# Optimization experiments

Measured on AMD Instinct MI355X. Metric: run time of the kernel, lower is better.

The kernel has to match this reference:

```python
import jax, jax.numpy as jnp
import numpy as np

GAMMA = 10.0  # params[('edge_penalty_gamma', 10.0, ...)]
EPS_SQRT = 1e-24  # guard for sqrt(0) (float_aware_sqrt)


def dXf(u, dx):
    # forward difference along axis -2, Neumann-zero boundary (replicate last row)
    return (jnp.concatenate([u[..., 1:, :], u[..., -1:, :]], axis=-2) - u) / dx


def dYf(u, dy):
    # forward difference along axis -1, Neumann-zero boundary (replicate last col)
    return (jnp.concatenate([u[..., :, 1:], u[..., :, -1:]], axis=-1) - u) / dy


def setup_inputs() -> dict:
    key = jax.random.key(0)
    k1, k2 = jax.random.split(key)
    B, K, H, W = 8, 8, 1024, 1024
    input_images = jax.random.normal(k1, (B, 1, H, W), dtype=jnp.float32)
    spacing = jnp.ones((2,), dtype=jnp.float32)
    label_probabilities = jax.random.uniform(k2, (B, K, H, W), dtype=jnp.float32)
    return {"input_images": input_images, "spacing": spacing,
            "label_probabilities": label_probabilities}


def reference(input_images, spacing, label_probabilities):
    # --- compute_localized_edge_penalty(I, spacing) ---
    I = input_images[:, 0, ...]                      # [B, H, W]
    sx, sy = spacing[0], spacing[1]
    gn2 = dXf(I, sx) ** 2 + dYf(I, sy) ** 2          # ||grad I||^2 (forward diffs)
    gnI = jnp.sqrt(jnp.maximum(gn2, EPS_SQRT))
    w_edge = 1.0 / (1.0 + GAMMA * gnI * jnp.min(spacing))  # [B, H, W]

    # --- normalized-cut relaxation over all clusters, fully batched ---
    p = label_probabilities                          # [B, K, H, W]
    # cut-cost stencil uses unit spacing (fd.FD_torch(spacing=[1.0]*dim))
    p_xp = dXf(p, 1.0)
    p_yp = dYf(p, 1.0)
    w = w_edge[:, None, :, :]                        # broadcast over clusters
    nom = jnp.sum(p * (p + w * (p_xp + p_yp)), axis=(-2, -1))   # [B, K]
    denom = jnp.sum(p * (1.0 + 2.0 * w), axis=(-2, -1))         # [B, K]
    cut_cost = nom / denom                                        # [B, K]

    B, K = p.shape[0], p.shape[1]
    current_penalties = K - jnp.sum(cut_cost, axis=1)            # [B]
    return jnp.sum(current_penalties)
```

## Files before the change

kernel.cpp:

```cpp
#include <hip/hip_runtime.h>


constexpr int Bsz  = 8;
constexpr int Kc   = 8;
constexpr int KPB  = 4;
constexpr int H    = 1024;
constexpr int W    = 1024;
constexpr int ROWS = 16;
constexpr int RB   = H / ROWS;
constexpr int TPB  = 256;

#define GAMMA_F    10.0f
#define EPS_SQRT_F 1e-24f

__device__ __forceinline__ float wedge(float c, float dn, float rt,
                                       float inv_sx, float inv_sy, float smin) {
    float dx = (dn - c) * inv_sx;
    float dy = (rt - c) * inv_sy;
    float gn2 = dx * dx + dy * dy;
    float g = sqrtf(fmaxf(gn2, EPS_SQRT_F));
    return 1.0f / (1.0f + GAMMA_F * g * smin);
}

__device__ __forceinline__ void accum(float pc, float pd, float pr, float w,
                                      float& nom, float& den) {
    float lap = (pd - pc) + (pr - pc);
    nom = fmaf(pc, fmaf(w, lap, pc), nom);
    den = fmaf(pc, fmaf(2.0f, w, 1.0f), den);
}

__global__ __launch_bounds__(TPB) void cl_main(const float* __restrict__ I,
                                               const float* __restrict__ spacing,
                                               const float* __restrict__ P,
                                               float2* __restrict__ ws) {
    const int t    = threadIdx.x;
    const int lane = t & 63;
    const int j0   = t * 4;
    const int b    = blockIdx.y;
    const int kh   = blockIdx.z;
    const int r0   = blockIdx.x * ROWS;

    const float sx = spacing[0], sy = spacing[1];
    const float inv_sx = 1.0f / sx, inv_sy = 1.0f / sy;
    const float smin = fminf(sx, sy);

    const int jr = (j0 + 4 < W) ? (j0 + 4) : (W - 1);
    const bool edge = (lane == 63);

    const float* Ib = I + (size_t)b * H * W;
    const float* Pk0 = P + ((size_t)(b * Kc + kh * KPB)) * H * W;

    float4 cI  = *(const float4*)(Ib + (size_t)r0 * W + j0);
    float  cIr = edge ? Ib[(size_t)r0 * W + jr] : 0.0f;
    float4 cp[KPB];
    float  cpr[KPB];
#pragma unroll
    for (int k = 0; k < KPB; ++k) {
        const float* Pk = Pk0 + (size_t)k * H * W;
        cp[k]  = *(const float4*)(Pk + (size_t)r0 * W + j0);
        cpr[k] = edge ? Pk[(size_t)r0 * W + jr] : 0.0f;
    }

    float nom[KPB], den[KPB];
#pragma unroll
    for (int k = 0; k < KPB; ++k) { nom[k] = 0.0f; den[k] = 0.0f; }

#pragma unroll 1
    for (int ii = 0; ii < ROWS; ++ii) {
        const int i = r0 + ii;
        const int inext = (i + 1 < H) ? (i + 1) : (H - 1);
        const size_t rn = (size_t)inext * W;

        const float4 nI  = *(const float4*)(Ib + rn + j0);
        const float  nIr = edge ? Ib[rn + jr] : 0.0f;

        float Irt = __shfl_down(cI.x, 1, 64);
        if (edge) Irt = cIr;

        const float w0 = wedge(cI.x, nI.x, cI.y, inv_sx, inv_sy, smin);
        const float w1 = wedge(cI.y, nI.y, cI.z, inv_sx, inv_sy, smin);
        const float w2 = wedge(cI.z, nI.z, cI.w, inv_sx, inv_sy, smin);
        const float w3 = wedge(cI.w, nI.w, Irt,  inv_sx, inv_sy, smin);

#pragma unroll
        for (int k = 0; k < KPB; ++k) {
            const float* Pk = Pk0 + (size_t)k * H * W;
            const float4 np  = *(const float4*)(Pk + rn + j0);
            const float  npr = edge ? Pk[rn + jr] : 0.0f;

            float prt = __shfl_down(cp[k].x, 1, 64);
            if (edge) prt = cpr[k];

            accum(cp[k].x, np.x, cp[k].y, w0, nom[k], den[k]);
            accum(cp[k].y, np.y, cp[k].z, w1, nom[k], den[k]);
            accum(cp[k].z, np.z, cp[k].w, w2, nom[k], den[k]);
            accum(cp[k].w, np.w, prt,     w3, nom[k], den[k]);

            cp[k]  = np;
            cpr[k] = npr;
        }
        cI  = nI;
        cIr = nIr;
    }

    __shared__ float red[4][2 * KPB];
    const int wave = t >> 6;

#pragma unroll
    for (int k = 0; k < KPB; ++k) {
        float n = nom[k], d = den[k];
#pragma unroll
        for (int off = 32; off > 0; off >>= 1) {
            n += __shfl_down(n, off, 64);
            d += __shfl_down(d, off, 64);
        }
        if (lane == 0) {
            red[wave][k]       = n;
            red[wave][KPB + k] = d;
        }
    }
    __syncthreads();

    if (t < KPB) {
        const int k = t;
        float n = red[0][k] + red[1][k] + red[2][k] + red[3][k];
        float d = red[0][KPB + k] + red[1][KPB + k] + red[2][KPB + k] + red[3][KPB + k];
        ws[(((size_t)(b * 2 + kh) * RB) + blockIdx.x) * KPB + k] = make_float2(n, d);
    }
}

__global__ __launch_bounds__(512) void cl_final(const float2* __restrict__ ws,
                                                float* __restrict__ out) {
    const int t    = threadIdx.x;
    const int acc  = t & 63;
    const int part = t >> 6;
    const int b = acc >> 3, k = acc & 7;
    const int kh = k >> 2, kk = k & 3;

    double n = 0.0, d = 0.0;
#pragma unroll
    for (int r = part; r < RB; r += 8) {
        const float2 v = ws[(((size_t)(b * 2 + kh) * RB) + r) * KPB + kk];
        n += (double)v.x;
        d += (double)v.y;
    }

    __shared__ double sn[64][8], sd[64][8];
    sn[acc][part] = n;
    sd[acc][part] = d;
    __syncthreads();

    if (t < 64) {
        double nn = 0.0, dd = 0.0;
#pragma unroll
        for (int p = 0; p < 8; ++p) { nn += sn[t][p]; dd += sd[t][p]; }
        double c = nn / dd;
#pragma unroll
        for (int off = 32; off > 0; off >>= 1) c += __shfl_down(c, off, 64);
        if (t == 0) out[0] = (float)((double)(Bsz * Kc) - c);
    }
}

extern "C" void kernel_launch(void* const* d_in, const int* in_sizes, int n_in,
                              void* d_out, int out_size, void* d_ws, size_t ws_size,
                              hipStream_t stream) {
    const float* I       = (const float*)d_in[0];
    const float* spacing = (const float*)d_in[1];
    const float* P       = (const float*)d_in[2];
    float* out = (float*)d_out;
    float2* ws = (float2*)d_ws;

    dim3 grid(RB, Bsz, 2);
    cl_main<<<grid, TPB, 0, stream>>>(I, spacing, P, ws);
    cl_final<<<1, 512, 0, stream>>>(ws, out);
}
```

Measured before the change: 383.0 us.

## Process all clusters per block and batch next-row loads

Each block now covers all eight clusters for its row strip instead of half, so the image rows and edge weights are loaded and computed once rather than twice. The next-row loads for every cluster are issued together before the accumulation, which raises the number of memory requests in flight. In exchange the grid is half as large and register pressure rises, which may lower occupancy.

```diff
diff --git a/kernel.cpp b/kernel.cpp
--- a/kernel.cpp
+++ b/kernel.cpp
@@ -3,7 +3,6 @@
 
 constexpr int Bsz  = 8;
 constexpr int Kc   = 8;
-constexpr int KPB  = 4;
 constexpr int H    = 1024;
 constexpr int W    = 1024;
 constexpr int ROWS = 16;
@@ -37,7 +36,6 @@
     const int lane = t & 63;
     const int j0   = t * 4;
     const int b    = blockIdx.y;
-    const int kh   = blockIdx.z;
     const int r0   = blockIdx.x * ROWS;
 
     const float sx = spacing[0], sy = spacing[1];
@@ -47,23 +45,23 @@
     const int jr = (j0 + 4 < W) ? (j0 + 4) : (W - 1);
     const bool edge = (lane == 63);
 
-    const float* Ib = I + (size_t)b * H * W;
-    const float* Pk0 = P + ((size_t)(b * Kc + kh * KPB)) * H * W;
+    const float* Ib  = I + (size_t)b * H * W;
+    const float* Pk0 = P + (size_t)b * Kc * H * W;
 
     float4 cI  = *(const float4*)(Ib + (size_t)r0 * W + j0);
     float  cIr = edge ? Ib[(size_t)r0 * W + jr] : 0.0f;
-    float4 cp[KPB];
-    float  cpr[KPB];
+    float4 cp[Kc];
+    float  cpr[Kc];
 #pragma unroll
-    for (int k = 0; k < KPB; ++k) {
+    for (int k = 0; k < Kc; ++k) {
         const float* Pk = Pk0 + (size_t)k * H * W;
         cp[k]  = *(const float4*)(Pk + (size_t)r0 * W + j0);
         cpr[k] = edge ? Pk[(size_t)r0 * W + jr] : 0.0f;
     }
 
-    float nom[KPB], den[KPB];
+    float nom[Kc], den[Kc];
 #pragma unroll
-    for (int k = 0; k < KPB; ++k) { nom[k] = 0.0f; den[k] = 0.0f; }
+    for (int k = 0; k < Kc; ++k) { nom[k] = 0.0f; den[k] = 0.0f; }
 
 #pragma unroll 1
     for (int ii = 0; ii < ROWS; ++ii) {
@@ -74,6 +72,15 @@
         const float4 nI  = *(const float4*)(Ib + rn + j0);
         const float  nIr = edge ? Ib[rn + jr] : 0.0f;
 
+        float4 np[Kc];
+        float  npr[Kc];
+#pragma unroll
+        for (int k = 0; k < Kc; ++k) {
+            const float* Pk = Pk0 + (size_t)k * H * W;
+            np[k]  = *(const float4*)(Pk + rn + j0);
+            npr[k] = edge ? Pk[rn + jr] : 0.0f;
+        }
+
         float Irt = __shfl_down(cI.x, 1, 64);
         if (edge) Irt = cIr;
 
@@ -83,31 +90,27 @@
         const float w3 = wedge(cI.w, nI.w, Irt,  inv_sx, inv_sy, smin);
 
 #pragma unroll
-        for (int k = 0; k < KPB; ++k) {
-            const float* Pk = Pk0 + (size_t)k * H * W;
-            const float4 np  = *(const float4*)(Pk + rn + j0);
-            const float  npr = edge ? Pk[rn + jr] : 0.0f;
-
+        for (int k = 0; k < Kc; ++k) {
             float prt = __shfl_down(cp[k].x, 1, 64);
             if (edge) prt = cpr[k];
 
-            accum(cp[k].x, np.x, cp[k].y, w0, nom[k], den[k]);
-            accum(cp[k].y, np.y, cp[k].z, w1, nom[k], den[k]);
-            accum(cp[k].z, np.z, cp[k].w, w2, nom[k], den[k]);
-            accum(cp[k].w, np.w, prt,     w3, nom[k], den[k]);
+            accum(cp[k].x, np[k].x, cp[k].y, w0, nom[k], den[k]);
+            accum(cp[k].y, np[k].y, cp[k].z, w1, nom[k], den[k]);
+            accum(cp[k].z, np[k].z, cp[k].w, w2, nom[k], den[k]);
+            accum(cp[k].w, np[k].w, prt,     w3, nom[k], den[k]);
 
-            cp[k]  = np;
-            cpr[k] = npr;
+            cp[k]  = np[k];
+            cpr[k] = npr[k];
         }
         cI  = nI;
         cIr = nIr;
     }
 
-    __shared__ float red[4][2 * KPB];
+    __shared__ float red[4][2 * Kc];
     const int wave = t >> 6;
 
 #pragma unroll
-    for (int k = 0; k < KPB; ++k) {
+    for (int k = 0; k < Kc; ++k) {
         float n = nom[k], d = den[k];
 #pragma unroll
         for (int off = 32; off > 0; off >>= 1) {
@@ -115,17 +118,17 @@
             d += __shfl_down(d, off, 64);
         }
         if (lane == 0) {
-            red[wave][k]       = n;
-            red[wave][KPB + k] = d;
+            red[wave][k]      = n;
+            red[wave][Kc + k] = d;
         }
     }
     __syncthreads();
 
-    if (t < KPB) {
+    if (t < Kc) {
         const int k = t;
         float n = red[0][k] + red[1][k] + red[2][k] + red[3][k];
-        float d = red[0][KPB + k] + red[1][KPB + k] + red[2][KPB + k] + red[3][KPB + k];
-        ws[(((size_t)(b * 2 + kh) * RB) + blockIdx.x) * KPB + k] = make_float2(n, d);
+        float d = red[0][Kc + k] + red[1][Kc + k] + red[2][Kc + k] + red[3][Kc + k];
+        ws[((size_t)b * RB + blockIdx.x) * Kc + k] = make_float2(n, d);
     }
 }
 
@@ -135,12 +138,11 @@
     const int acc  = t & 63;
     const int part = t >> 6;
     const int b = acc >> 3, k = acc & 7;
-    const int kh = k >> 2, kk = k & 3;
 
     double n = 0.0, d = 0.0;
 #pragma unroll
     for (int r = part; r < RB; r += 8) {
-        const float2 v = ws[(((size_t)(b * 2 + kh) * RB) + r) * KPB + kk];
+        const float2 v = ws[((size_t)b * RB + r) * Kc + k];
         n += (double)v.x;
         d += (double)v.y;
     }
@@ -170,7 +172,7 @@
     float* out = (float*)d_out;
     float2* ws = (float2*)d_ws;
 
-    dim3 grid(RB, Bsz, 2);
+    dim3 grid(RB, Bsz);
     cl_main<<<grid, TPB, 0, stream>>>(I, spacing, P, ws);
     cl_final<<<1, 512, 0, stream>>>(ws, out);
 }
```

After: 384.8 us. About the same (+0.5%).
